# Performance work log

Measured on AMD Instinct MI355X. Metric: run time of the kernel, lower is better.

Reference implementation:

```python
import jax, jax.numpy as jnp
import numpy as np

T, B, LAG, H = 128, 1024, 6, 256


def setup_inputs() -> dict:
    key = jax.random.key(0)
    ks = jax.random.split(key, 16)
    s = 0.05  # small init scale to keep LSTM gates in a sane range
    d = {}
    d["x"] = jax.random.normal(ks[0], (T, B, LAG), jnp.float32)
    d["Wi1"] = jax.random.normal(ks[1], (H, LAG), jnp.float32) * s
    d["bi1"] = jnp.zeros((H,), jnp.float32)
    d["Wi2"] = jax.random.normal(ks[2], (H, H), jnp.float32) * s
    d["bi2"] = jnp.zeros((H,), jnp.float32)
    d["Wi3"] = jax.random.normal(ks[3], (H, H), jnp.float32) * s
    d["bi3"] = jnp.zeros((H,), jnp.float32)
    d["Wih0"] = jax.random.normal(ks[4], (4 * H, H), jnp.float32) * s
    d["Whh0"] = jax.random.normal(ks[5], (4 * H, H), jnp.float32) * s
    d["bih0"] = jnp.zeros((4 * H,), jnp.float32)
    d["bhh0"] = jnp.zeros((4 * H,), jnp.float32)
    d["Wih1"] = jax.random.normal(ks[6], (4 * H, H), jnp.float32) * s
    d["Whh1"] = jax.random.normal(ks[7], (4 * H, H), jnp.float32) * s
    d["bih1"] = jnp.zeros((4 * H,), jnp.float32)
    d["bhh1"] = jnp.zeros((4 * H,), jnp.float32)
    d["Wo1"] = jax.random.normal(ks[8], (H, H), jnp.float32) * s
    d["bo1"] = jnp.zeros((H,), jnp.float32)
    d["Wo2"] = jax.random.normal(ks[9], (H, H), jnp.float32) * s
    d["bo2"] = jnp.zeros((H,), jnp.float32)
    d["Wo3"] = jax.random.normal(ks[10], (LAG, H), jnp.float32) * s
    d["bo3"] = jnp.zeros((LAG,), jnp.float32)
    return d


def _lstm_cell(xt, h, c, Wih, Whh, bih, bhh):
    # PyTorch gate order: i, f, g, o
    g = xt @ Wih.T + h @ Whh.T + (bih + bhh)
    i, f, gg, o = jnp.split(g, 4, axis=-1)
    c2 = jax.nn.sigmoid(f) * c + jax.nn.sigmoid(i) * jnp.tanh(gg)
    h2 = jax.nn.sigmoid(o) * jnp.tanh(c2)
    return h2, c2


def reference(x, Wi1, bi1, Wi2, bi2, Wi3, bi3,
              Wih0, Whh0, bih0, bhh0, Wih1, Whh1, bih1, bhh1,
              Wo1, bo1, Wo2, bo2, Wo3, bo3):
    relu = jax.nn.relu
    # input MLP applied to every timestep at once: [T,B,6] -> [T,B,H]
    u = relu(x @ Wi1.T + bi1)
    u = relu(u @ Wi2.T + bi2)
    u = relu(u @ Wi3.T + bi3)

    def step(carry, xt):
        h0, c0, h1, c1 = carry
        h0, c0 = _lstm_cell(xt, h0, c0, Wih0, Whh0, bih0, bhh0)
        # dropout(0.05) between layers is identity in eval mode
        h1, c1 = _lstm_cell(h0, h1, c1, Wih1, Whh1, bih1, bhh1)
        return (h0, c0, h1, c1), h1

    z = jnp.zeros((x.shape[1], Whh0.shape[1]), x.dtype)
    _, hs = jax.lax.scan(step, (z, z, z, z), u)  # hs: [T,B,H]

    # output MLP: ReLU, Linear, ReLU, Linear, ReLU, Linear(H->6)
    y = relu(hs)
    y = relu(y @ Wo1.T + bo1)
    y = relu(y @ Wo2.T + bo2)
    y = y @ Wo3.T + bo3
    return y  # [T,B,6]
```

## Files before the change

kernel.cpp:

```cpp
#include <hip/hip_runtime.h>
#include <math.h>


namespace {
constexpr int kT   = 128;
constexpr int kB   = 1024;
constexpr int kLag = 6;
constexpr int kH   = 256;
constexpr int kTc  = 32;
constexpr int kMc  = kTc * kB;
constexpr int kGS  = 67;
constexpr int kLdsForce = 98304;
}

typedef _Float16 half8 __attribute__((ext_vector_type(8)));
typedef _Float16 half2 __attribute__((ext_vector_type(2)));
typedef float f32x4 __attribute__((ext_vector_type(4)));
typedef unsigned long long u64;

__device__ __forceinline__ float sigm(float x) {
    return 1.f / (1.f + exp2f(-1.4426950408889634f * x));
}
__device__ __forceinline__ float tanh_(float x) {
    return 2.f / (1.f + exp2f(-2.8853900817779268f * x)) - 1.f;
}

__device__ __forceinline__ half8 pack(u64 a, u64 b) {
    union { u64 u[2]; half8 h; } r;
    r.u[0] = a; r.u[1] = b;
    return r.h;
}

__device__ __forceinline__ void ld_l2(half8& d, const _Float16* p) {
    asm volatile("global_load_dwordx4 %0, %1, off sc0"
                 : "=v"(d) : "v"(p) : "memory");
}
__device__ __forceinline__ void ld_pln(half8& d, const _Float16* p) {
    asm volatile("global_load_dwordx4 %0, %1, off"
                 : "=v"(d) : "v"(p) : "memory");
}
__device__ __forceinline__ void atomic_add_nr(unsigned int* p, unsigned int v) {
    asm volatile("global_atomic_add %0, %1, off"
                 :: "v"(p), "v"(v) : "memory");
}
__device__ __forceinline__ unsigned int atomic_rd(unsigned int* p) {
    unsigned int d;
    unsigned int z = 0u;
    asm volatile("global_atomic_add %0, %1, %2, off sc0\n\ts_waitcnt vmcnt(0)"
                 : "=v"(d) : "v"(p), "v"(z) : "memory");
    return d;
}
#define WAITCNT_HOLD16(A)                                                     \
    asm volatile("s_waitcnt vmcnt(0)"                                         \
        : "+v"(A[0]), "+v"(A[1]), "+v"(A[2]), "+v"(A[3]),                     \
          "+v"(A[4]), "+v"(A[5]), "+v"(A[6]), "+v"(A[7]),                     \
          "+v"(A[8]), "+v"(A[9]), "+v"(A[10]), "+v"(A[11]),                   \
          "+v"(A[12]), "+v"(A[13]), "+v"(A[14]), "+v"(A[15]))

__global__ __launch_bounds__(256)
void zero_fill(unsigned int* __restrict__ p)
{
    p[blockIdx.x * 256 + threadIdx.x] = 0u;
}

__global__ __launch_bounds__(256)
void cvt_f2h(const float* __restrict__ s, _Float16* __restrict__ d)
{
    const int i = blockIdx.x * 256 + threadIdx.x;
    d[i] = (_Float16)s[i];
}

__global__ __launch_bounds__(256)
void build_wcat(const float* __restrict__ Wih, const float* __restrict__ Whh,
                _Float16* __restrict__ d)
{
    const int i = blockIdx.x * 256 + threadIdx.x;
    const int row = i >> 9, col = i & 511;
    const float v = (col < 256) ? Wih[row * 256 + col] : Whh[row * 256 + col - 256];
    d[i] = (_Float16)v;
}

__global__ __launch_bounds__(256)
void add_bias(const float* __restrict__ a, const float* __restrict__ b,
              float* __restrict__ d)
{
    const int i = blockIdx.x * 256 + threadIdx.x;
    d[i] = a[i] + b[i];
}

__global__ __launch_bounds__(256)
void in_mlp1(const float* __restrict__ x, const float* __restrict__ Wi1,
             const float* __restrict__ bi1, _Float16* __restrict__ out)
{
    const int idx = blockIdx.x * 256 + threadIdx.x;
    const int col = idx & (kH - 1);
    const int row = idx >> 8;
    const float* xr = x + (size_t)row * kLag;
    const float* w  = Wi1 + col * kLag;
    float s = bi1[col];
#pragma unroll
    for (int k = 0; k < kLag; ++k) s = fmaf(xr[k], w[k], s);
    out[idx] = (_Float16)fmaxf(s, 0.f);
}

__global__ __launch_bounds__(256)
void gemm_h16(const _Float16* __restrict__ A, const _Float16* __restrict__ W,
              const float* __restrict__ bias, _Float16* __restrict__ C)
{
    const int tid = threadIdx.x;
    const int w = tid >> 6, lane = tid & 63, q = lane >> 4, l15 = lane & 15;
    const int n0 = blockIdx.x * 64;
    const int r0 = blockIdx.y * 128 + w * 32;

    half8 bf[4][8];
#pragma unroll
    for (int nt = 0; nt < 4; ++nt)
#pragma unroll
        for (int kk = 0; kk < 8; ++kk)
            bf[nt][kk] = *(const half8*)(W + (size_t)(n0 + nt * 16 + l15) * 256
                                         + kk * 32 + q * 8);
    float bz[4];
#pragma unroll
    for (int nt = 0; nt < 4; ++nt) bz[nt] = bias[n0 + nt * 16 + l15];

#pragma unroll
    for (int rt = 0; rt < 2; ++rt) {
        const _Float16* arow = A + (size_t)(r0 + rt * 16 + l15) * 256 + q * 8;
        half8 af[8];
#pragma unroll
        for (int kk = 0; kk < 8; ++kk) af[kk] = *(const half8*)(arow + kk * 32);
        f32x4 acc[4];
#pragma unroll
        for (int nt = 0; nt < 4; ++nt)
            acc[nt] = (f32x4){bz[nt], bz[nt], bz[nt], bz[nt]};
#pragma unroll
        for (int kk = 0; kk < 8; ++kk)
#pragma unroll
            for (int nt = 0; nt < 4; ++nt)
                acc[nt] = __builtin_amdgcn_mfma_f32_16x16x32_f16(
                    af[kk], bf[nt][kk], acc[nt], 0, 0, 0);
#pragma unroll
        for (int nt = 0; nt < 4; ++nt)
#pragma unroll
            for (int r = 0; r < 4; ++r) {
                const float v = fmaxf(acc[nt][r], 0.f);
                C[(size_t)(r0 + rt * 16 + q * 4 + r) * 256 + n0 + nt * 16 + l15]
                    = (_Float16)v;
            }
    }
}

__device__ __forceinline__ void xbar(unsigned int* __restrict__ cptr,
                                     unsigned int target, int tid)
{
    asm volatile("s_waitcnt vmcnt(0)" ::: "memory");
    __syncthreads();
    if (tid == 0) {
        atomic_add_nr(cptr, 1u);
        while (atomic_rd(cptr) < target)
            __builtin_amdgcn_s_sleep(1);
    }
    __syncthreads();
}

__device__ __forceinline__ void gather_lo(const _Float16* lo, int row, int q,
                                          u64* ua)
{
    const u64* plo = (const u64*)(lo + (size_t)row * 256 + q * 8);
#pragma unroll
    for (int kk = 0; kk < 8; ++kk) {
        ua[2*kk]   = plo[kk*8];
        ua[2*kk+1] = plo[kk*8 + 1];
    }
}

__device__ __forceinline__ void gstore(float* __restrict__ gl, int m0, int nb,
                                       int q, int l15,
                                       const f32x4& a0, const f32x4& a1)
{
#pragma unroll
    for (int r = 0; r < 4; ++r) {
        gl[(m0 + q*4 + r) * kGS + nb + l15]      = a0[r];
        gl[(m0 + q*4 + r) * kGS + nb + 16 + l15] = a1[r];
    }
}

template<bool CLO>
__device__ __forceinline__ void phase_gemm(
    const _Float16* __restrict__ lo, const _Float16* __restrict__ hi,
    const half8 (&B0)[16], const half8 (&B1)[16],
    float* __restrict__ gl, int rtb, int nb, int q, int l15)
{
#pragma unroll
    for (int rt = 0; rt < 2; ++rt) {
        const int row = (rtb + rt) * 16 + l15;
        const _Float16* plo = lo + (size_t)row * 256 + q * 8;
        const _Float16* phi = hi + (size_t)row * 256 + q * 8;
        half8 A[16];
#pragma unroll
        for (int kk = 0; kk < 8; ++kk) {
            if (CLO) ld_l2(A[kk], plo + kk * 32);
            else     ld_pln(A[kk], plo + kk * 32);
            ld_l2(A[8 + kk], phi + kk * 32);
        }
        WAITCNT_HOLD16(A);
        f32x4 a0 = {0.f,0.f,0.f,0.f}, a1 = {0.f,0.f,0.f,0.f};
#pragma unroll
        for (int kk = 0; kk < 16; ++kk) {
            a0 = __builtin_amdgcn_mfma_f32_16x16x32_f16(A[kk], B0[kk], a0, 0,0,0);
            a1 = __builtin_amdgcn_mfma_f32_16x16x32_f16(A[kk], B1[kk], a1, 0,0,0);
        }
        gstore(gl, (rtb + rt) * 16, nb, q, l15, a0, a1);
    }
}

__device__ __forceinline__ void cell_one(const float* __restrict__ gl,
    int crow, int cc, const float* __restrict__ bs, float* __restrict__ cst,
    _Float16* __restrict__ hout, _Float16* __restrict__ uout)
{
    const float* gr = gl + crow * kGS;
    _Float16 hp[2];
#pragma unroll
    for (int e = 0; e < 2; ++e) {
        const float gi = gr[0*16 + cc + e] + bs[e*4 + 0];
        const float gf = gr[1*16 + cc + e] + bs[e*4 + 1];
        const float gg = gr[2*16 + cc + e] + bs[e*4 + 2];
        const float go = gr[3*16 + cc + e] + bs[e*4 + 3];
        const float c2 = sigm(gf) * cst[e] + sigm(gi) * tanh_(gg);
        cst[e] = c2;
        hp[e] = (_Float16)(sigm(go) * tanh_(c2));
    }
    *(half2*)(hout + (size_t)crow * 256 + cc) = (half2){hp[0], hp[1]};
    if (uout) {
        const _Float16 z = (_Float16)0.f;
        *(half2*)(uout + (size_t)crow * 256 + cc) =
            (half2){hp[0] > z ? hp[0] : z, hp[1] > z ? hp[1] : z};
    }
}

__global__ __launch_bounds__(512, 2)
void lstm_all(_Float16* __restrict__ ubuf,
              const _Float16* __restrict__ Wc0, const _Float16* __restrict__ Wc1,
              const float* __restrict__ bc0, const float* __restrict__ bc1,
              _Float16* __restrict__ h0b, _Float16* __restrict__ h1b,
              unsigned int* __restrict__ cnt)
{
    extern __shared__ char lds[];
    float* gl0 = (float*)lds;
    float* gl1 = gl0 + 64 * kGS;

    const int tid = threadIdx.x;
    const int w = tid >> 6, lane = tid & 63, q = lane >> 4, l15 = lane & 15;
    const int wl = w & 3;
    const int rtb = (wl >> 1) * 2;
    const int nb  = (wl & 1) * 32;
    const int lyr = (w < 4) ? 1 : 0;

    __shared__ int sh_bi, sh_js;
    if (tid == 0) {
        unsigned int xcd = __builtin_amdgcn_s_getreg(20 | (31 << 11)) & 7u;
        unsigned int rank = __hip_atomic_fetch_add(cnt + 512 + xcd * 16, 1u,
            __ATOMIC_RELAXED, __HIP_MEMORY_SCOPE_AGENT);
        sh_bi = (int)(xcd * 2 + (rank >> 4));
        sh_js = (int)(rank & 15);
    }
    __syncthreads();
    const int bi = sh_bi, js = sh_js;
    unsigned int* cptr = cnt + bi * 32;

    const _Float16* WcL = lyr ? Wc1 : Wc0;
    half8 Bf0[16], Bf1[16];
    {
        const _Float16* wr0 = WcL
            + (size_t)((nb >> 4) * 256 + js * 16 + l15) * 512 + q * 8;
        const _Float16* wr1 = WcL
            + (size_t)(((nb >> 4) + 1) * 256 + js * 16 + l15) * 512 + q * 8;
#pragma unroll
        for (int kk = 0; kk < 16; ++kk) {
            Bf0[kk] = *(const half8*)(wr0 + kk * 32);
            Bf1[kk] = *(const half8*)(wr1 + kk * 32);
        }
    }

    const int cc = (tid & 7) * 2;
    const int crow = tid >> 3;
    float bs0[8], bs1[8];
#pragma unroll
    for (int e = 0; e < 2; ++e)
#pragma unroll
        for (int g = 0; g < 4; ++g) {
            bs0[e*4 + g] = bc0[g * 256 + js * 16 + cc + e];
            bs1[e*4 + g] = bc1[g * 256 + js * 16 + cc + e];
        }
    float cst0[2] = {0.f, 0.f}, cst1[2] = {0.f, 0.f};
    const size_t rbase = (size_t)bi * 64 * 256;
    const size_t obase = rbase + js * 16;

    if (lyr == 0) {
#pragma unroll
        for (int rt = 0; rt < 2; ++rt) {
            u64 ua[16];
            gather_lo(ubuf + rbase, (rtb + rt) * 16 + l15, q, ua);
            f32x4 a0 = {0.f,0.f,0.f,0.f}, a1 = {0.f,0.f,0.f,0.f};
#pragma unroll
            for (int kk = 0; kk < 8; ++kk) {
                const half8 af = pack(ua[2*kk], ua[2*kk+1]);
                a0 = __builtin_amdgcn_mfma_f32_16x16x32_f16(af, Bf0[kk], a0, 0,0,0);
                a1 = __builtin_amdgcn_mfma_f32_16x16x32_f16(af, Bf1[kk], a1, 0,0,0);
            }
            gstore(gl0, (rtb + rt) * 16, nb, q, l15, a0, a1);
        }
    }
    __syncthreads();
    cell_one(gl0, crow, cc, bs0, cst0, h0b + obase, nullptr);
    xbar(cptr, 16u, tid);

    for (int t = 0; t < kT; ++t) {
        const size_t p  = (size_t)(t & 1) * kB * 256;
        const size_t pn = (size_t)((t & 1) ^ 1) * kB * 256;
        const bool hasB = (t < kT - 1);
        if (lyr == 1) {
            phase_gemm<true>(h0b + p + rbase, h1b + pn + rbase,
                             Bf0, Bf1, gl1, rtb, nb, q, l15);
        } else if (hasB) {
            phase_gemm<false>(ubuf + (size_t)(t + 1) * kB * 256 + rbase,
                              h0b + p + rbase,
                              Bf0, Bf1, gl0, rtb, nb, q, l15);
        }
        __syncthreads();
        cell_one(gl1, crow, cc, bs1, cst1, h1b + p + obase,
                 ubuf + (size_t)t * kB * 256 + obase);
        if (hasB) {
            cell_one(gl0, crow, cc, bs0, cst0, h0b + pn + obase, nullptr);
            xbar(cptr, (unsigned)(16 * (t + 2)), tid);
        }
    }
}

__global__ __launch_bounds__(256)
void out_mlp3(const _Float16* __restrict__ y2, const float* __restrict__ Wo3,
              const float* __restrict__ bo3, float* __restrict__ out)
{
    const int lane = threadIdx.x & 63;
    const int row  = blockIdx.x * 4 + (threadIdx.x >> 6);
    const _Float16* yr = y2 + (size_t)row * kH + lane * 4;
    const float a0 = (float)yr[0], a1 = (float)yr[1], a2 = (float)yr[2], a3 = (float)yr[3];
    float s[kLag];
#pragma unroll
    for (int o = 0; o < kLag; ++o) {
        const float4 wv = *(const float4*)(Wo3 + o * kH + lane * 4);
        s[o] = a0 * wv.x + a1 * wv.y + a2 * wv.z + a3 * wv.w;
    }
#pragma unroll
    for (int off = 32; off > 0; off >>= 1) {
#pragma unroll
        for (int o = 0; o < kLag; ++o) s[o] += __shfl_down(s[o], off);
    }
    if (lane == 0) {
#pragma unroll
        for (int o = 0; o < kLag; ++o)
            out[(size_t)row * kLag + o] = s[o] + bo3[o];
    }
}

extern "C" void kernel_launch(void* const* d_in, const int* in_sizes, int n_in,
                              void* d_out, int out_size, void* d_ws, size_t ws_size,
                              hipStream_t stream)
{
    const float* x    = (const float*)d_in[0];
    const float* Wi1  = (const float*)d_in[1];
    const float* bi1  = (const float*)d_in[2];
    const float* Wi2  = (const float*)d_in[3];
    const float* bi2  = (const float*)d_in[4];
    const float* Wi3  = (const float*)d_in[5];
    const float* bi3  = (const float*)d_in[6];
    const float* Wih0 = (const float*)d_in[7];
    const float* Whh0 = (const float*)d_in[8];
    const float* bih0 = (const float*)d_in[9];
    const float* bhh0 = (const float*)d_in[10];
    const float* Wih1 = (const float*)d_in[11];
    const float* Whh1 = (const float*)d_in[12];
    const float* bih1 = (const float*)d_in[13];
    const float* bhh1 = (const float*)d_in[14];
    const float* Wo1  = (const float*)d_in[15];
    const float* bo1  = (const float*)d_in[16];
    const float* Wo2  = (const float*)d_in[17];
    const float* bo2  = (const float*)d_in[18];
    const float* Wo3  = (const float*)d_in[19];
    const float* bo3  = (const float*)d_in[20];
    float* outp = (float*)d_out;

    char* p = (char*)d_ws;
    _Float16* ubuf = (_Float16*)p;  p += (size_t)kT * kB * kH * 2;
    _Float16* s1   = (_Float16*)p;  p += (size_t)kMc * kH * 2;
    _Float16* s2   = (_Float16*)p;  p += (size_t)kMc * kH * 2;
    _Float16* Wc0  = (_Float16*)p;  p += (size_t)1024 * 512 * 2;
    _Float16* Wc1  = (_Float16*)p;  p += (size_t)1024 * 512 * 2;
    _Float16* W2h  = (_Float16*)p;  p += (size_t)kH * kH * 2;
    _Float16* W3h  = (_Float16*)p;  p += (size_t)kH * kH * 2;
    _Float16* Wo1h = (_Float16*)p;  p += (size_t)kH * kH * 2;
    _Float16* Wo2h = (_Float16*)p;  p += (size_t)kH * kH * 2;
    float* bc0 = (float*)p;  p += 1024 * 4;
    float* bc1 = (float*)p;  p += 1024 * 4;
    _Float16* h0b = (_Float16*)p;  p += (size_t)2 * kB * kH * 2;
    _Float16* h1b = (_Float16*)p;  p += (size_t)2 * kB * kH * 2;
    unsigned int* cnt = (unsigned int*)p;  p += 4096;

    zero_fill<<<2052, 256, 0, stream>>>((unsigned int*)h0b);
    cvt_f2h<<<kH * kH / 256, 256, 0, stream>>>(Wi2, W2h);
    cvt_f2h<<<kH * kH / 256, 256, 0, stream>>>(Wi3, W3h);
    cvt_f2h<<<kH * kH / 256, 256, 0, stream>>>(Wo1, Wo1h);
    cvt_f2h<<<kH * kH / 256, 256, 0, stream>>>(Wo2, Wo2h);
    build_wcat<<<1024 * 512 / 256, 256, 0, stream>>>(Wih0, Whh0, Wc0);
    build_wcat<<<1024 * 512 / 256, 256, 0, stream>>>(Wih1, Whh1, Wc1);
    add_bias<<<4, 256, 0, stream>>>(bih0, bhh0, bc0);
    add_bias<<<4, 256, 0, stream>>>(bih1, bhh1, bc1);

    for (int c = 0; c < kT / kTc; ++c) {
        in_mlp1<<<kMc * kH / 256, 256, 0, stream>>>(
            x + (size_t)c * kMc * kLag, Wi1, bi1, s1);
        gemm_h16<<<dim3(4, kMc / 128), 256, 0, stream>>>(s1, W2h, bi2, s2);
        gemm_h16<<<dim3(4, kMc / 128), 256, 0, stream>>>(
            s2, W3h, bi3, ubuf + (size_t)c * kMc * kH);
    }

    static bool attr_set = false;
    if (!attr_set) {
        hipFuncSetAttribute((const void*)lstm_all,
                            hipFuncAttributeMaxDynamicSharedMemorySize, kLdsForce);
        attr_set = true;
    }
    void* args[] = {&ubuf, &Wc0, &Wc1, &bc0, &bc1, &h0b, &h1b, &cnt};
    hipLaunchCooperativeKernel((const void*)lstm_all, dim3(256), dim3(512),
                               args, kLdsForce, stream);

    for (int c = 0; c < kT / kTc; ++c) {
        gemm_h16<<<dim3(4, kMc / 128), 256, 0, stream>>>(
            ubuf + (size_t)c * kMc * kH, Wo1h, bo1, s1);
        gemm_h16<<<dim3(4, kMc / 128), 256, 0, stream>>>(s1, Wo2h, bo2, s2);
        out_mlp3<<<kMc / 4, 256, 0, stream>>>(
            s2, Wo3, bo3, outp + (size_t)c * kMc * kLag);
    }
}
```

Before: 1.984 ms.

## Overlap next-step input-projection GEMM with grid barrier wait in LSTM

Layer-0 blocks now compute the u(t+2)·Wih part of the gate pre-activation while waiting at the cross-block barrier. The per-step critical path is left with only the h·Whh half. The barrier is split into an arrive phase and a wait phase so this work fills the spin time. Separately, the MLP chunk size doubles and the scratch buffers are reused in place to drop one buffer. The costs are more live accumulator registers across the loop and a larger chunk footprint.

```diff
diff --git a/kernel.cpp b/kernel.cpp
--- a/kernel.cpp
+++ b/kernel.cpp
@@ -7,7 +7,7 @@
 constexpr int kB   = 1024;
 constexpr int kLag = 6;
 constexpr int kH   = 256;
-constexpr int kTc  = 32;
+constexpr int kTc  = 64;
 constexpr int kMc  = kTc * kB;
 constexpr int kGS  = 67;
 constexpr int kLdsForce = 98304;
@@ -23,12 +23,6 @@
 }
 __device__ __forceinline__ float tanh_(float x) {
     return 2.f / (1.f + exp2f(-2.8853900817779268f * x)) - 1.f;
-}
-
-__device__ __forceinline__ half8 pack(u64 a, u64 b) {
-    union { u64 u[2]; half8 h; } r;
-    r.u[0] = a; r.u[1] = b;
-    return r.h;
 }
 
 __device__ __forceinline__ void ld_l2(half8& d, const _Float16* p) {
@@ -50,6 +44,10 @@
                  : "=v"(d) : "v"(p), "v"(z) : "memory");
     return d;
 }
+#define WAITCNT_HOLD8(A)                                                      \
+    asm volatile("s_waitcnt vmcnt(0)"                                         \
+        : "+v"(A[0]), "+v"(A[1]), "+v"(A[2]), "+v"(A[3]),                     \
+          "+v"(A[4]), "+v"(A[5]), "+v"(A[6]), "+v"(A[7]))
 #define WAITCNT_HOLD16(A)                                                     \
     asm volatile("s_waitcnt vmcnt(0)"                                         \
         : "+v"(A[0]), "+v"(A[1]), "+v"(A[2]), "+v"(A[3]),                     \
@@ -150,30 +148,6 @@
     }
 }
 
-__device__ __forceinline__ void xbar(unsigned int* __restrict__ cptr,
-                                     unsigned int target, int tid)
-{
-    asm volatile("s_waitcnt vmcnt(0)" ::: "memory");
-    __syncthreads();
-    if (tid == 0) {
-        atomic_add_nr(cptr, 1u);
-        while (atomic_rd(cptr) < target)
-            __builtin_amdgcn_s_sleep(1);
-    }
-    __syncthreads();
-}
-
-__device__ __forceinline__ void gather_lo(const _Float16* lo, int row, int q,
-                                          u64* ua)
-{
-    const u64* plo = (const u64*)(lo + (size_t)row * 256 + q * 8);
-#pragma unroll
-    for (int kk = 0; kk < 8; ++kk) {
-        ua[2*kk]   = plo[kk*8];
-        ua[2*kk+1] = plo[kk*8 + 1];
-    }
-}
-
 __device__ __forceinline__ void gstore(float* __restrict__ gl, int m0, int nb,
                                        int q, int l15,
                                        const f32x4& a0, const f32x4& a1)
@@ -185,8 +159,7 @@
     }
 }
 
-template<bool CLO>
-__device__ __forceinline__ void phase_gemm(
+__device__ __forceinline__ void phase_gemm_l1(
     const _Float16* __restrict__ lo, const _Float16* __restrict__ hi,
     const half8 (&B0)[16], const half8 (&B1)[16],
     float* __restrict__ gl, int rtb, int nb, int q, int l15)
@@ -199,8 +172,7 @@
         half8 A[16];
 #pragma unroll
         for (int kk = 0; kk < 8; ++kk) {
-            if (CLO) ld_l2(A[kk], plo + kk * 32);
-            else     ld_pln(A[kk], plo + kk * 32);
+            ld_l2(A[kk], plo + kk * 32);
             ld_l2(A[8 + kk], phi + kk * 32);
         }
         WAITCNT_HOLD16(A);
@@ -211,6 +183,56 @@
             a1 = __builtin_amdgcn_mfma_f32_16x16x32_f16(A[kk], B1[kk], a1, 0,0,0);
         }
         gstore(gl, (rtb + rt) * 16, nb, q, l15, a0, a1);
+    }
+}
+
+__device__ __forceinline__ void prework_u(
+    const _Float16* __restrict__ lo,
+    const half8 (&B0)[16], const half8 (&B1)[16],
+    int rtb, int q, int l15, f32x4 (&acc)[2][2])
+{
+#pragma unroll
+    for (int rt = 0; rt < 2; ++rt) {
+        const int row = (rtb + rt) * 16 + l15;
+        const _Float16* plo = lo + (size_t)row * 256 + q * 8;
+        half8 A[8];
+#pragma unroll
+        for (int kk = 0; kk < 8; ++kk) ld_pln(A[kk], plo + kk * 32);
+        WAITCNT_HOLD8(A);
+        acc[rt][0] = (f32x4){0.f,0.f,0.f,0.f};
+        acc[rt][1] = (f32x4){0.f,0.f,0.f,0.f};
+#pragma unroll
+        for (int kk = 0; kk < 8; ++kk) {
+            acc[rt][0] = __builtin_amdgcn_mfma_f32_16x16x32_f16(
+                A[kk], B0[kk], acc[rt][0], 0,0,0);
+            acc[rt][1] = __builtin_amdgcn_mfma_f32_16x16x32_f16(
+                A[kk], B1[kk], acc[rt][1], 0,0,0);
+        }
+    }
+}
+
+__device__ __forceinline__ void finish_h(
+    const _Float16* __restrict__ hi,
+    const half8 (&B0)[16], const half8 (&B1)[16],
+    float* __restrict__ gl, int rtb, int nb, int q, int l15,
+    f32x4 (&acc)[2][2])
+{
+#pragma unroll
+    for (int rt = 0; rt < 2; ++rt) {
+        const int row = (rtb + rt) * 16 + l15;
+        const _Float16* phi = hi + (size_t)row * 256 + q * 8;
+        half8 A[8];
+#pragma unroll
+        for (int kk = 0; kk < 8; ++kk) ld_l2(A[kk], phi + kk * 32);
+        WAITCNT_HOLD8(A);
+#pragma unroll
+        for (int kk = 0; kk < 8; ++kk) {
+            acc[rt][0] = __builtin_amdgcn_mfma_f32_16x16x32_f16(
+                A[kk], B0[8 + kk], acc[rt][0], 0,0,0);
+            acc[rt][1] = __builtin_amdgcn_mfma_f32_16x16x32_f16(
+                A[kk], B1[8 + kk], acc[rt][1], 0,0,0);
+        }
+        gstore(gl, (rtb + rt) * 16, nb, q, l15, acc[rt][0], acc[rt][1]);
     }
 }
 
@@ -296,43 +318,52 @@
     const size_t rbase = (size_t)bi * 64 * 256;
     const size_t obase = rbase + js * 16;
 
+    f32x4 accB[2][2];
+
     if (lyr == 0) {
-#pragma unroll
-        for (int rt = 0; rt < 2; ++rt) {
-            u64 ua[16];
-            gather_lo(ubuf + rbase, (rtb + rt) * 16 + l15, q, ua);
-            f32x4 a0 = {0.f,0.f,0.f,0.f}, a1 = {0.f,0.f,0.f,0.f};
-#pragma unroll
-            for (int kk = 0; kk < 8; ++kk) {
-                const half8 af = pack(ua[2*kk], ua[2*kk+1]);
-                a0 = __builtin_amdgcn_mfma_f32_16x16x32_f16(af, Bf0[kk], a0, 0,0,0);
-                a1 = __builtin_amdgcn_mfma_f32_16x16x32_f16(af, Bf1[kk], a1, 0,0,0);
-            }
-            gstore(gl0, (rtb + rt) * 16, nb, q, l15, a0, a1);
-        }
+        prework_u(ubuf + rbase, Bf0, Bf1, rtb, q, l15, accB);
+        gstore(gl0, rtb * 16, nb, q, l15, accB[0][0], accB[0][1]);
+        gstore(gl0, (rtb + 1) * 16, nb, q, l15, accB[1][0], accB[1][1]);
     }
     __syncthreads();
     cell_one(gl0, crow, cc, bs0, cst0, h0b + obase, nullptr);
-    xbar(cptr, 16u, tid);
+    asm volatile("s_waitcnt vmcnt(0)" ::: "memory");
+    __syncthreads();
+    if (tid == 0) atomic_add_nr(cptr, 1u);
+    if (lyr == 0)
+        prework_u(ubuf + (size_t)1 * kB * 256 + rbase, Bf0, Bf1,
+                  rtb, q, l15, accB);
+    if (tid == 0) {
+        while (atomic_rd(cptr) < 16u) __builtin_amdgcn_s_sleep(1);
+    }
+    __syncthreads();
 
     for (int t = 0; t < kT; ++t) {
         const size_t p  = (size_t)(t & 1) * kB * 256;
         const size_t pn = (size_t)((t & 1) ^ 1) * kB * 256;
         const bool hasB = (t < kT - 1);
         if (lyr == 1) {
-            phase_gemm<true>(h0b + p + rbase, h1b + pn + rbase,
-                             Bf0, Bf1, gl1, rtb, nb, q, l15);
+            phase_gemm_l1(h0b + p + rbase, h1b + pn + rbase,
+                          Bf0, Bf1, gl1, rtb, nb, q, l15);
         } else if (hasB) {
-            phase_gemm<false>(ubuf + (size_t)(t + 1) * kB * 256 + rbase,
-                              h0b + p + rbase,
-                              Bf0, Bf1, gl0, rtb, nb, q, l15);
+            finish_h(h0b + p + rbase, Bf0, Bf1, gl0, rtb, nb, q, l15, accB);
         }
         __syncthreads();
         cell_one(gl1, crow, cc, bs1, cst1, h1b + p + obase,
                  ubuf + (size_t)t * kB * 256 + obase);
         if (hasB) {
             cell_one(gl0, crow, cc, bs0, cst0, h0b + pn + obase, nullptr);
-            xbar(cptr, (unsigned)(16 * (t + 2)), tid);
+            asm volatile("s_waitcnt vmcnt(0)" ::: "memory");
+            __syncthreads();
+            if (tid == 0) atomic_add_nr(cptr, 1u);
+            if (lyr == 0 && t < kT - 2)
+                prework_u(ubuf + (size_t)(t + 2) * kB * 256 + rbase,
+                          Bf0, Bf1, rtb, q, l15, accB);
+            if (tid == 0) {
+                const unsigned int tgt = (unsigned)(16 * (t + 2));
+                while (atomic_rd(cptr) < tgt) __builtin_amdgcn_s_sleep(1);
+            }
+            __syncthreads();
         }
     }
 }
@@ -393,7 +424,6 @@
     char* p = (char*)d_ws;
     _Float16* ubuf = (_Float16*)p;  p += (size_t)kT * kB * kH * 2;
     _Float16* s1   = (_Float16*)p;  p += (size_t)kMc * kH * 2;
-    _Float16* s2   = (_Float16*)p;  p += (size_t)kMc * kH * 2;
     _Float16* Wc0  = (_Float16*)p;  p += (size_t)1024 * 512 * 2;
     _Float16* Wc1  = (_Float16*)p;  p += (size_t)1024 * 512 * 2;
     _Float16* W2h  = (_Float16*)p;  p += (size_t)kH * kH * 2;
@@ -417,11 +447,11 @@
     add_bias<<<4, 256, 0, stream>>>(bih1, bhh1, bc1);
 
     for (int c = 0; c < kT / kTc; ++c) {
+        _Float16* ub = ubuf + (size_t)c * kMc * kH;
         in_mlp1<<<kMc * kH / 256, 256, 0, stream>>>(
-            x + (size_t)c * kMc * kLag, Wi1, bi1, s1);
-        gemm_h16<<<dim3(4, kMc / 128), 256, 0, stream>>>(s1, W2h, bi2, s2);
-        gemm_h16<<<dim3(4, kMc / 128), 256, 0, stream>>>(
-            s2, W3h, bi3, ubuf + (size_t)c * kMc * kH);
+            x + (size_t)c * kMc * kLag, Wi1, bi1, ub);
+        gemm_h16<<<dim3(4, kMc / 128), 256, 0, stream>>>(ub, W2h, bi2, s1);
+        gemm_h16<<<dim3(4, kMc / 128), 256, 0, stream>>>(s1, W3h, bi3, ub);
     }
 
     static bool attr_set = false;
@@ -435,10 +465,10 @@
                                args, kLdsForce, stream);
 
     for (int c = 0; c < kT / kTc; ++c) {
-        gemm_h16<<<dim3(4, kMc / 128), 256, 0, stream>>>(
-            ubuf + (size_t)c * kMc * kH, Wo1h, bo1, s1);
-        gemm_h16<<<dim3(4, kMc / 128), 256, 0, stream>>>(s1, Wo2h, bo2, s2);
+        _Float16* ub = ubuf + (size_t)c * kMc * kH;
+        gemm_h16<<<dim3(4, kMc / 128), 256, 0, stream>>>(ub, Wo1h, bo1, s1);
+        gemm_h16<<<dim3(4, kMc / 128), 256, 0, stream>>>(s1, Wo2h, bo2, ub);
         out_mlp3<<<kMc / 4, 256, 0, stream>>>(
-            s2, Wo3, bo3, outp + (size_t)c * kMc * kLag);
-    }
-}
+            ub, Wo3, bo3, outp + (size_t)c * kMc * kLag);
+    }
+}
```

New measurement: 1.989 ms. Within noise of the previous version (+0.2%).
